# Optimization experiments

Hardware: AMD Instinct MI355X
Metric: run time of the kernel (lower is better)

Reference implementation:

```python
import jax, jax.numpy as jnp
import numpy as np

B = 8192       # batch (tokens)
D = 2048       # data_dim
DEPTH = 3      # tree depth: 1 root + 2 mid + 4 leaf experts
INIT = 0.02


def setup_inputs() -> dict:
    key = jax.random.key(0)
    ks = jax.random.split(key, 6)
    x = jax.random.normal(ks[0], (B, D), dtype=jnp.float32)
    # router output simulated as i.i.d. path bits (router is a frozen pretrained black box)
    path_mask = jax.random.randint(ks[1], (B, DEPTH), 0, 2, dtype=jnp.int32)
    W0 = jax.random.normal(ks[2], (D, D), dtype=jnp.float32) * INIT
    b0 = jnp.zeros((D,), dtype=jnp.float32)
    W1 = jax.random.normal(ks[3], (2, D, D), dtype=jnp.float32) * INIT  # depth-1 experts
    b1 = jnp.zeros((2, D), dtype=jnp.float32)
    W2 = jax.random.normal(ks[4], (4, D, D), dtype=jnp.float32) * INIT  # depth-2 (leaf) experts
    b2 = jnp.zeros((4, D), dtype=jnp.float32)
    return {"x": x, "W0": W0, "b0": b0, "W1": W1, "b1": b1,
            "W2": W2, "b2": b2, "path_mask": path_mask}


def reference(x, W0, b0, W1, b1, W2, b2, path_mask):
    # Root expert (depth 0): applied to all tokens.
    h0 = jax.nn.relu(x @ W0 + b0)                                  # [B, D]
    bit0 = path_mask[:, 0]                                          # routes depth-1 children
    bit1 = path_mask[:, 1]                                          # routes depth-2 children
    # Depth-1: 2 experts; dense compute then per-token select (static-shape MoE dispatch).
    h1_all = jax.nn.relu(jnp.einsum('bd,edf->bef', h0, W1) + b1)    # [B, 2, D]
    h1 = jnp.take_along_axis(h1_all, bit0[:, None, None].astype(jnp.int32), axis=1)[:, 0]
    # Depth-2 (leaves): 4 experts indexed by the 2-bit path.
    leaf = 2 * bit0 + bit1                                          # [B] in {0,1,2,3}
    h2_all = jax.nn.relu(jnp.einsum('bd,edf->bef', h1, W2) + b2)    # [B, 4, D]
    y = jnp.take_along_axis(h2_all, leaf[:, None, None].astype(jnp.int32), axis=1)[:, 0]
    return y
```

## Files before the change

kernel.cpp:

```cpp
#include <hip/hip_runtime.h>

#define BB 8192
#define DD 2048
#define NSLOT 7
#define NP1 (BB + 2*128)
#define NP2 (BB + 4*128)

typedef unsigned short u16;
typedef unsigned int   u32;
typedef unsigned long long u64;

typedef __bf16 bf16x8 __attribute__((ext_vector_type(8)));
typedef float  f32x4  __attribute__((ext_vector_type(4)));
typedef u16    u16x8  __attribute__((ext_vector_type(8)));

#define OFF_WT   0ull
#define OFF_XB   (OFF_WT + (size_t)NSLOT*DD*DD*2)
#define OFF_H0   (OFF_XB + (size_t)BB*DD*2)
#define OFF_P1   (OFF_H0 + (size_t)BB*DD*2)
#define OFF_P2   (OFF_P1 + (size_t)NP1*4)
#define OFF_META (OFF_P2 + (size_t)NP2*4)

__device__ __forceinline__ u16 f2bf(float f) {
  u32 u = __float_as_uint(f);
  u32 r = (u + 0x7FFFu + ((u >> 16) & 1u)) >> 16;
  return (u16)r;
}
__device__ __forceinline__ float bf2f(u16 u) {
  return __uint_as_float(((u32)u) << 16);
}

__device__ __forceinline__ void gld16(const void* g, void* l) {
  __builtin_amdgcn_global_load_lds(
      (const __attribute__((address_space(1))) void*)g,
      (__attribute__((address_space(3))) void*)l, 16, 0, 0);
}


__global__ void k_detect(const u16* x, int* meta) {
  __shared__ int cnt, cntz;
  if (threadIdx.x == 0) { cnt = 0; cntz = 0; }
  __syncthreads();
  u16 u = x[threadIdx.x * 17];
  int ex = (u >> 7) & 0xFF;
  int sane = (ex == 0) || (ex >= 112 && ex <= 143);
  atomicAdd(&cnt, sane);
  atomicAdd(&cntz, (u == 0) ? 1 : 0);
  __syncthreads();
  if (threadIdx.x == 0) meta[20] = (cnt >= 205 && cntz < 64) ? 1 : 0;
}

__global__ __launch_bounds__(1024) void k_route(const int* __restrict__ pm,
                                                int* __restrict__ p1,
                                                int* __restrict__ p2,
                                                int* __restrict__ meta) {
  __shared__ int cnt[6];
  __shared__ int cur[6];
  __shared__ int base1[2], base2[4];
  const int tid = threadIdx.x;
  const int lane = tid & 63;
  if (tid < 6) { cnt[tid] = 0; cur[tid] = 0; }
  __syncthreads();

  for (int i = tid; i < NP1; i += 1024) p1[i] = -1;
  for (int i = tid; i < NP2; i += 1024) p2[i] = -1;

  int myb0[8], myleaf[8];
  #pragma unroll
  for (int i = 0; i < 8; ++i) {
    int b = i * 1024 + tid;
    int b0 = pm[b*3] & 1, b1 = pm[b*3+1] & 1;
    myb0[i] = b0; myleaf[i] = b0*2 + b1;
  }
  #pragma unroll
  for (int i = 0; i < 8; ++i) {
    u64 m0 = __ballot(myb0[i] == 0);
    if (lane == 0) {
      atomicAdd(&cnt[0], __popcll(m0));
      atomicAdd(&cnt[1], 64 - __popcll(m0));
    }
    #pragma unroll
    for (int e = 0; e < 4; ++e) {
      u64 me = __ballot(myleaf[i] == e);
      if (lane == 0) atomicAdd(&cnt[2+e], __popcll(me));
    }
  }
  __syncthreads();
  if (tid == 0) {
    base1[0] = 0;
    base1[1] = (cnt[0] + 127) & ~127;
    meta[12] = 0; meta[13] = base1[1];
    meta[14] = base1[1] + ((cnt[1] + 127) & ~127);
    int b = 0;
    #pragma unroll
    for (int e = 0; e < 4; ++e) {
      base2[e] = b; meta[15+e] = b;
      b += (cnt[2+e] + 127) & ~127;
    }
    meta[19] = b;
  }
  __syncthreads();
  #pragma unroll
  for (int i = 0; i < 8; ++i) {
    int b = i * 1024 + tid;
    u64 lt = (1ull << lane) - 1ull;
    #pragma unroll
    for (int g = 0; g < 2; ++g) {
      u64 m = __ballot(myb0[i] == g);
      int pos = __popcll(m & lt);
      int wbase = 0;
      if (lane == 0 && m) wbase = atomicAdd(&cur[g], __popcll(m));
      wbase = __shfl(wbase, 0);
      if (myb0[i] == g) p1[base1[g] + wbase + pos] = b;
    }
    #pragma unroll
    for (int g = 0; g < 4; ++g) {
      u64 m = __ballot(myleaf[i] == g);
      int pos = __popcll(m & lt);
      int wbase = 0;
      if (lane == 0 && m) wbase = atomicAdd(&cur[2+g], __popcll(m));
      wbase = __shfl(wbase, 0);
      if (myleaf[i] == g) p2[base2[g] + wbase + pos] = b;
    }
  }
}

__global__ void k_cvtx(const void* __restrict__ x, u16* __restrict__ xb,
                       const int* __restrict__ meta) {
  int i = blockIdx.x * 256 + threadIdx.x;
  if (meta[20]) {
    ((uint4*)xb)[i] = ((const uint4*)x)[i];
  } else {
    const float4* p = (const float4*)x + (size_t)i * 2;
    float4 a = p[0], b = p[1];
    uint4 o;
    o.x = f2bf(a.x) | ((u32)f2bf(a.y) << 16);
    o.y = f2bf(a.z) | ((u32)f2bf(a.w) << 16);
    o.z = f2bf(b.x) | ((u32)f2bf(b.y) << 16);
    o.w = f2bf(b.z) | ((u32)f2bf(b.w) << 16);
    ((uint4*)xb)[i] = o;
  }
}

__global__ void k_wt(const void* __restrict__ W0, const void* __restrict__ W1,
                     const void* __restrict__ W2, u16* __restrict__ wt,
                     const int* __restrict__ meta) {
  __shared__ u16 tile[64][66];
  int bid = blockIdx.x;
  int slot = bid >> 10;
  int t = bid & 1023;
  int tr = t >> 5, tc = t & 31;
  const void* src; size_t eoff;
  if (slot == 0)      { src = W0; eoff = 0; }
  else if (slot <= 2) { src = W1; eoff = (size_t)(slot-1)*DD*DD; }
  else                { src = W2; eoff = (size_t)(slot-3)*DD*DD; }
  int r0 = tr*64, c0 = tc*64;
  int tid = threadIdx.x;
  int isbf = meta[20];
  #pragma unroll
  for (int i = 0; i < 4; ++i) {
    int idx = tid + i*256;
    int r = idx >> 4, c4 = (idx & 15) * 4;
    size_t goff = eoff + (size_t)(r0 + r)*DD + c0 + c4;
    u16 v0, v1, v2, v3;
    if (isbf) {
      ushort4 v = *(const ushort4*)((const u16*)src + goff);
      v0 = v.x; v1 = v.y; v2 = v.z; v3 = v.w;
    } else {
      float4 v = *(const float4*)((const float*)src + goff);
      v0 = f2bf(v.x); v1 = f2bf(v.y); v2 = f2bf(v.z); v3 = f2bf(v.w);
    }
    tile[r][c4+0] = v0; tile[r][c4+1] = v1;
    tile[r][c4+2] = v2; tile[r][c4+3] = v3;
  }
  __syncthreads();
  u16* dst = wt + (size_t)slot*DD*DD;
  #pragma unroll
  for (int i = 0; i < 2; ++i) {
    int idx = tid + i*256;
    int n = idx >> 3, j = idx & 7;
    u16x8 o;
    #pragma unroll
    for (int k = 0; k < 8; ++k) o[k] = tile[j*8 + k][n];
    *(u16x8*)&dst[(size_t)(c0 + n)*DD + r0 + j*8] = o;
  }
}

__global__ __launch_bounds__(256, 2) void k_gemm(
    const u16* __restrict__ A, const u16* __restrict__ Wt,
    const void* __restrict__ bias, const int* __restrict__ perm,
    const int* __restrict__ bases, int nexp,
    void* __restrict__ Out, int final_out, const int* __restrict__ meta) {
  __shared__ __align__(16) u16 As[128*32];
  __shared__ __align__(16) u16 Bs[128*32];

  const int tid  = threadIdx.x;
  const int wid  = tid >> 6;
  const int lane = tid & 63;
  const int m0 = blockIdx.y * 128;
  const int n0 = blockIdx.x * 128;

  int e = 0;
  if (nexp == 2)      e = (m0 >= bases[1]);
  else if (nexp == 4) e = (m0 >= bases[1]) + (m0 >= bases[2]) + (m0 >= bases[3]);
  const u16* W = Wt + (size_t)e * DD * DD;

  const u16* gA[2]; const u16* gB[2];
  u16* lA[2]; u16* lB[2];
  #pragma unroll
  for (int p = 0; p < 2; ++p) {
    int seg   = p*4 + wid;
    int boff  = seg*1024 + lane*16;
    int row   = boff >> 6;
    int chunk = (boff >> 4) & 3;
    int kk    = (chunk ^ ((row >> 1) & 3)) * 8;
    int gr = m0 + row;
    if (perm) { int t = perm[gr]; gr = (t < 0) ? 0 : t; }
    gA[p] = A + (size_t)gr * DD + kk;
    gB[p] = W + (size_t)(n0 + row) * DD + kk;
    lA[p] = (u16*)((char*)As + seg*1024);
    lB[p] = (u16*)((char*)Bs + seg*1024);
  }

  f32x4 zero = {0.0f, 0.0f, 0.0f, 0.0f};
  f32x4 acc[4][4];
  #pragma unroll
  for (int i = 0; i < 4; ++i)
    #pragma unroll
    for (int j = 0; j < 4; ++j) acc[i][j] = zero;

  const int wm = wid & 1, wn = wid >> 1;
  const int q = lane >> 4, cl = lane & 15;
  const int sw = q ^ ((cl >> 1) & 3);
  const int aoff  = (wm*64 + cl) * 32 + sw*8;
  const int boff2 = (wn*64 + cl) * 32 + sw*8;

  for (int k0 = 0; k0 < DD; k0 += 32) {
    gld16(gA[0] + k0, lA[0]);
    gld16(gA[1] + k0, lA[1]);
    gld16(gB[0] + k0, lB[0]);
    gld16(gB[1] + k0, lB[1]);
    __syncthreads();
    bf16x8 af[4], bf[4];
    #pragma unroll
    for (int mt = 0; mt < 4; ++mt) af[mt] = *(const bf16x8*)&As[aoff + mt*16*32];
    #pragma unroll
    for (int nt = 0; nt < 4; ++nt) bf[nt] = *(const bf16x8*)&Bs[boff2 + nt*16*32];
    #pragma unroll
    for (int mt = 0; mt < 4; ++mt)
      #pragma unroll
      for (int nt = 0; nt < 4; ++nt)
        acc[mt][nt] = __builtin_amdgcn_mfma_f32_16x16x32_bf16(af[mt], bf[nt], acc[mt][nt], 0, 0, 0);
    __syncthreads();
  }

  const int isbf = meta[20];
  float bv[4];
  #pragma unroll
  for (int nt = 0; nt < 4; ++nt) {
    int col = n0 + wn*64 + nt*16 + cl;
    bv[nt] = isbf ? bf2f(((const u16*)bias)[e*DD + col])
                  : ((const float*)bias)[e*DD + col];
  }
  #pragma unroll
  for (int mt = 0; mt < 4; ++mt) {
    int rbase = m0 + wm*64 + mt*16 + q*4;
    #pragma unroll
    for (int r = 0; r < 4; ++r) {
      int row = rbase + r;
      int orow = row;
      if (perm) { orow = perm[row]; if (orow < 0) continue; }
      #pragma unroll
      for (int nt = 0; nt < 4; ++nt) {
        int col = n0 + wn*64 + nt*16 + cl;
        float v = acc[mt][nt][r] + bv[nt];
        v = v > 0.0f ? v : 0.0f;
        if (!final_out || isbf) ((u16*)Out)[(size_t)orow*DD + col] = f2bf(v);
        else                    ((float*)Out)[(size_t)orow*DD + col] = v;
      }
    }
  }
}

extern "C" void kernel_launch(void* const* d_in, const int* in_sizes, int n_in,
                              void* d_out, int out_size, void* d_ws, size_t ws_size,
                              hipStream_t stream) {
  (void)in_sizes; (void)n_in; (void)out_size; (void)ws_size;
  const void* x  = d_in[0];
  const void* W0 = d_in[1];
  const void* b0 = d_in[2];
  const void* W1 = d_in[3];
  const void* b1 = d_in[4];
  const void* W2 = d_in[5];
  const void* b2 = d_in[6];
  const int*  pm = (const int*)d_in[7];

  char* ws  = (char*)d_ws;
  u16*  wt  = (u16*)(ws + OFF_WT);
  u16*  xb  = (u16*)(ws + OFF_XB);
  u16*  h0  = (u16*)(ws + OFF_H0);
  u16*  h1  = xb;
  int*  p1  = (int*)(ws + OFF_P1);
  int*  p2  = (int*)(ws + OFF_P2);
  int*  meta= (int*)(ws + OFF_META);

  hipLaunchKernelGGL(k_detect, dim3(1),  dim3(256),  0, stream, (const u16*)x, meta);
  hipLaunchKernelGGL(k_route,  dim3(1),  dim3(1024), 0, stream, pm, p1, p2, meta);
  hipLaunchKernelGGL(k_cvtx,   dim3(BB*DD/8/256), dim3(256), 0, stream, x, xb, meta);
  hipLaunchKernelGGL(k_wt,     dim3(7*1024), dim3(256), 0, stream, W0, W1, W2, wt, meta);

  hipLaunchKernelGGL(k_gemm, dim3(16, 64), dim3(256), 0, stream,
                     xb, wt, b0, (const int*)nullptr, (const int*)nullptr, 1,
                     (void*)h0, 0, meta);
  hipLaunchKernelGGL(k_gemm, dim3(16, 66), dim3(256), 0, stream,
                     h0, wt + (size_t)1*DD*DD, b1, p1, meta + 12, 2,
                     (void*)h1, 0, meta);
  hipLaunchKernelGGL(k_gemm, dim3(16, 68), dim3(256), 0, stream,
                     h1, wt + (size_t)3*DD*DD, b2, p2, meta + 15, 4,
                     d_out, 1, meta);
}
```

Before: 554.2 us.

## Rewrite expert GEMM with 256x128 tiles, 4-stage LDS pipeline, and XCD swizzle

Replaces the single-buffered 128x128 GEMM with a 512-thread, 256x128-tile kernel. It uses a 4-deep async global-to-LDS ring with vmcnt-based waits, so loads run ahead of the MFMAs and each step needs fewer barriers. It also remaps workgroup IDs to group tiles per XCD for better L2 reuse, and returns early on fully padded row tiles. Routing padding becomes 256-aligned, which adds more padding rows per expert, and the LDS layout drops the XOR swizzle, which may bring bank conflicts.

```diff
diff --git a/kernel.cpp b/kernel.cpp
--- a/kernel.cpp
+++ b/kernel.cpp
@@ -3,8 +3,8 @@
 #define BB 8192
 #define DD 2048
 #define NSLOT 7
-#define NP1 (BB + 2*128)
-#define NP2 (BB + 4*128)
+#define NP1 (BB + 2*256)
+#define NP2 (BB + 4*256)
 
 typedef unsigned short u16;
 typedef unsigned int   u32;
@@ -88,14 +88,14 @@
   __syncthreads();
   if (tid == 0) {
     base1[0] = 0;
-    base1[1] = (cnt[0] + 127) & ~127;
+    base1[1] = (cnt[0] + 255) & ~255;
     meta[12] = 0; meta[13] = base1[1];
-    meta[14] = base1[1] + ((cnt[1] + 127) & ~127);
+    meta[14] = base1[1] + ((cnt[1] + 255) & ~255);
     int b = 0;
     #pragma unroll
     for (int e = 0; e < 4; ++e) {
       base2[e] = b; meta[15+e] = b;
-      b += (cnt[2+e] + 127) & ~127;
+      b += (cnt[2+e] + 255) & ~255;
     }
     meta[19] = b;
   }
@@ -186,41 +186,77 @@
   }
 }
 
-__global__ __launch_bounds__(256, 2) void k_gemm(
+#define SBA(T) ((u32)(((T) & 3) * 24576))
+#define SBB(T) ((u32)(((T) & 3) * 24576 + 16384))
+
+#define TILE(T, STAGE, VMN) do {                                             \
+  asm volatile("s_waitcnt vmcnt(" #VMN ")" ::: "memory");                    \
+  __builtin_amdgcn_s_barrier();                                              \
+  {                                                                          \
+    if (STAGE) {                                                             \
+      const int t3 = (T) + 3;                                                \
+      gld16(gA0 + (size_t)t3 * 32, sm + SBA(t3) + wid * 1024);               \
+      gld16(gA1 + (size_t)t3 * 32, sm + SBA(t3) + 8192 + wid * 1024);        \
+      gld16(gB0 + (size_t)t3 * 32, sm + SBB(t3) + wid * 1024);               \
+    }                                                                        \
+    const u32 sa = SBA(T) + aoff;                                            \
+    const u32 sb = SBB(T) + boff;                                            \
+    bf16x8 af[4], bfr[4];                                                    \
+    _Pragma("unroll") for (int mt = 0; mt < 4; ++mt)                         \
+      af[mt] = *(const bf16x8*)(sm + sa + mt * 1024);                        \
+    _Pragma("unroll") for (int nt = 0; nt < 4; ++nt)                         \
+      bfr[nt] = *(const bf16x8*)(sm + sb + nt * 1024);                       \
+    asm volatile("s_waitcnt lgkmcnt(0)" ::: "memory");                       \
+    __builtin_amdgcn_sched_barrier(0);                                       \
+    __builtin_amdgcn_s_setprio(1);                                           \
+    _Pragma("unroll") for (int mt = 0; mt < 4; ++mt)                         \
+      _Pragma("unroll") for (int nt = 0; nt < 4; ++nt)                       \
+        acc[mt][nt] = __builtin_amdgcn_mfma_f32_16x16x32_bf16(               \
+            af[mt], bfr[nt], acc[mt][nt], 0, 0, 0);                          \
+    __builtin_amdgcn_s_setprio(0);                                           \
+    __builtin_amdgcn_s_barrier();                                            \
+  }                                                                          \
+} while (0)
+
+__global__ __launch_bounds__(512, 2) void k_gemm(
     const u16* __restrict__ A, const u16* __restrict__ Wt,
     const void* __restrict__ bias, const int* __restrict__ perm,
     const int* __restrict__ bases, int nexp,
     void* __restrict__ Out, int final_out, const int* __restrict__ meta) {
-  __shared__ __align__(16) u16 As[128*32];
-  __shared__ __align__(16) u16 Bs[128*32];
+  __shared__ __align__(16) char sm[4 * 24576];
 
   const int tid  = threadIdx.x;
   const int wid  = tid >> 6;
   const int lane = tid & 63;
-  const int m0 = blockIdx.y * 128;
-  const int n0 = blockIdx.x * 128;
+
+  const u32 nwg = gridDim.x * gridDim.y;
+  const u32 wg  = blockIdx.y * gridDim.x + blockIdx.x;
+  const u32 cpx = nwg >> 3;
+  const u32 swz = (wg & 7u) * cpx + (wg >> 3);
+  const int m0 = (int)(swz >> 4) * 256;
+  const int n0 = (int)(swz & 15u) * 128;
 
   int e = 0;
   if (nexp == 2)      e = (m0 >= bases[1]);
   else if (nexp == 4) e = (m0 >= bases[1]) + (m0 >= bases[2]) + (m0 >= bases[3]);
+  if (perm && m0 >= bases[nexp]) return;
   const u16* W = Wt + (size_t)e * DD * DD;
 
-  const u16* gA[2]; const u16* gB[2];
-  u16* lA[2]; u16* lB[2];
-  #pragma unroll
-  for (int p = 0; p < 2; ++p) {
-    int seg   = p*4 + wid;
-    int boff  = seg*1024 + lane*16;
-    int row   = boff >> 6;
-    int chunk = (boff >> 4) & 3;
-    int kk    = (chunk ^ ((row >> 1) & 3)) * 8;
-    int gr = m0 + row;
-    if (perm) { int t = perm[gr]; gr = (t < 0) ? 0 : t; }
-    gA[p] = A + (size_t)gr * DD + kk;
-    gB[p] = W + (size_t)(n0 + row) * DD + kk;
-    lA[p] = (u16*)((char*)As + seg*1024);
-    lB[p] = (u16*)((char*)Bs + seg*1024);
-  }
+  const int sr = wid * 16 + (lane >> 2);
+  const int kc = (lane & 3) * 8;
+  int ar0 = m0 + sr, ar1 = m0 + 128 + sr;
+  if (perm) {
+    int v0 = perm[ar0]; ar0 = v0 < 0 ? 0 : v0;
+    int v1 = perm[ar1]; ar1 = v1 < 0 ? 0 : v1;
+  }
+  const u16* gA0 = A + (size_t)ar0 * DD + kc;
+  const u16* gA1 = A + (size_t)ar1 * DD + kc;
+  const u16* gB0 = W + (size_t)(n0 + sr) * DD + kc;
+
+  const int wm = wid >> 1, wn = wid & 1;
+  const int q = lane >> 4, cl = lane & 15;
+  const u32 aoff = (u32)((wm * 64 + cl) * 64 + q * 16);
+  const u32 boff = (u32)((wn * 64 + cl) * 64 + q * 16);
 
   f32x4 zero = {0.0f, 0.0f, 0.0f, 0.0f};
   f32x4 acc[4][4];
@@ -229,42 +265,30 @@
     #pragma unroll
     for (int j = 0; j < 4; ++j) acc[i][j] = zero;
 
-  const int wm = wid & 1, wn = wid >> 1;
-  const int q = lane >> 4, cl = lane & 15;
-  const int sw = q ^ ((cl >> 1) & 3);
-  const int aoff  = (wm*64 + cl) * 32 + sw*8;
-  const int boff2 = (wn*64 + cl) * 32 + sw*8;
-
-  for (int k0 = 0; k0 < DD; k0 += 32) {
-    gld16(gA[0] + k0, lA[0]);
-    gld16(gA[1] + k0, lA[1]);
-    gld16(gB[0] + k0, lB[0]);
-    gld16(gB[1] + k0, lB[1]);
-    __syncthreads();
-    bf16x8 af[4], bf[4];
-    #pragma unroll
-    for (int mt = 0; mt < 4; ++mt) af[mt] = *(const bf16x8*)&As[aoff + mt*16*32];
-    #pragma unroll
-    for (int nt = 0; nt < 4; ++nt) bf[nt] = *(const bf16x8*)&Bs[boff2 + nt*16*32];
-    #pragma unroll
-    for (int mt = 0; mt < 4; ++mt)
-      #pragma unroll
-      for (int nt = 0; nt < 4; ++nt)
-        acc[mt][nt] = __builtin_amdgcn_mfma_f32_16x16x32_bf16(af[mt], bf[nt], acc[mt][nt], 0, 0, 0);
-    __syncthreads();
-  }
+  #pragma unroll
+  for (int tt = 0; tt < 3; ++tt) {
+    gld16(gA0 + (size_t)tt * 32, sm + SBA(tt) + wid * 1024);
+    gld16(gA1 + (size_t)tt * 32, sm + SBA(tt) + 8192 + wid * 1024);
+    gld16(gB0 + (size_t)tt * 32, sm + SBB(tt) + wid * 1024);
+  }
+
+  #pragma unroll 1
+  for (int t = 0; t < 61; ++t) TILE(t, true, 6);
+  TILE(61, false, 6);
+  TILE(62, false, 3);
+  TILE(63, false, 0);
 
   const int isbf = meta[20];
   float bv[4];
   #pragma unroll
   for (int nt = 0; nt < 4; ++nt) {
-    int col = n0 + wn*64 + nt*16 + cl;
-    bv[nt] = isbf ? bf2f(((const u16*)bias)[e*DD + col])
-                  : ((const float*)bias)[e*DD + col];
+    int col = n0 + wn * 64 + nt * 16 + cl;
+    bv[nt] = isbf ? bf2f(((const u16*)bias)[e * DD + col])
+                  : ((const float*)bias)[e * DD + col];
   }
   #pragma unroll
   for (int mt = 0; mt < 4; ++mt) {
-    int rbase = m0 + wm*64 + mt*16 + q*4;
+    int rbase = m0 + wm * 64 + mt * 16 + q * 4;
     #pragma unroll
     for (int r = 0; r < 4; ++r) {
       int row = rbase + r;
@@ -272,15 +296,19 @@
       if (perm) { orow = perm[row]; if (orow < 0) continue; }
       #pragma unroll
       for (int nt = 0; nt < 4; ++nt) {
-        int col = n0 + wn*64 + nt*16 + cl;
+        int col = n0 + wn * 64 + nt * 16 + cl;
         float v = acc[mt][nt][r] + bv[nt];
         v = v > 0.0f ? v : 0.0f;
-        if (!final_out || isbf) ((u16*)Out)[(size_t)orow*DD + col] = f2bf(v);
-        else                    ((float*)Out)[(size_t)orow*DD + col] = v;
+        if (!final_out || isbf) ((u16*)Out)[(size_t)orow * DD + col] = f2bf(v);
+        else                    ((float*)Out)[(size_t)orow * DD + col] = v;
       }
     }
   }
 }
+
+#undef TILE
+#undef SBA
+#undef SBB
 
 extern "C" void kernel_launch(void* const* d_in, const int* in_sizes, int n_in,
                               void* d_out, int out_size, void* d_ws, size_t ws_size,
@@ -309,13 +337,13 @@
   hipLaunchKernelGGL(k_cvtx,   dim3(BB*DD/8/256), dim3(256), 0, stream, x, xb, meta);
   hipLaunchKernelGGL(k_wt,     dim3(7*1024), dim3(256), 0, stream, W0, W1, W2, wt, meta);
 
-  hipLaunchKernelGGL(k_gemm, dim3(16, 64), dim3(256), 0, stream,
+  hipLaunchKernelGGL(k_gemm, dim3(16, 32), dim3(512), 0, stream,
                      xb, wt, b0, (const int*)nullptr, (const int*)nullptr, 1,
                      (void*)h0, 0, meta);
-  hipLaunchKernelGGL(k_gemm, dim3(16, 66), dim3(256), 0, stream,
+  hipLaunchKernelGGL(k_gemm, dim3(16, NP1/256), dim3(512), 0, stream,
                      h0, wt + (size_t)1*DD*DD, b1, p1, meta + 12, 2,
                      (void*)h1, 0, meta);
-  hipLaunchKernelGGL(k_gemm, dim3(16, 68), dim3(256), 0, stream,
+  hipLaunchKernelGGL(k_gemm, dim3(16, NP2/256), dim3(512), 0, stream,
                      h1, wt + (size_t)3*DD*DD, b2, p2, meta + 15, 4,
                      d_out, 1, meta);
 }
```

Measured after the change: 558.2 us. No clear change (+0.7%).
